# Kernel optimization log

Measured on AMD Instinct MI355X. Metric: run time of the kernel, lower is better.

The kernel has to match this reference:

```python
import jax, jax.numpy as jnp
import numpy as np

N_ATOMS = 15000
N_EDGES = 300000
F = 128          # n_atom_basis
L = 3            # n_interactions
N_RBF = 20
CUTOFF = 5.0
MAX_Z = 100


def setup_inputs() -> dict:
    key = jax.random.key(0)
    ks = jax.random.split(key, 20)

    atomic_numbers = jax.random.randint(ks[0], (N_ATOMS,), 1, MAX_Z)
    # relative position vectors; norms roughly within cutoff
    r_ij = jax.random.normal(ks[1], (N_EDGES, 3), dtype=jnp.float32) * 1.5
    idx_i = jax.random.randint(ks[2], (N_EDGES,), 0, N_ATOMS)
    idx_j = jax.random.randint(ks[3], (N_EDGES,), 0, N_ATOMS)

    def lin(k, fan_in, shape):
        return (jax.random.normal(k, shape, dtype=jnp.float32) / np.sqrt(fan_in)).astype(jnp.float32)

    embedding = lin(ks[4], F, (MAX_Z, F)).at[0].set(0.0)  # padding_idx=0
    filt_W = lin(ks[5], N_RBF, (N_RBF, L * 3 * F))
    filt_b = jnp.zeros((L * 3 * F,), jnp.float32)

    inter_W1 = lin(ks[6], F, (L, F, F));        inter_b1 = jnp.zeros((L, F), jnp.float32)
    inter_W2 = lin(ks[7], F, (L, F, 3 * F));    inter_b2 = jnp.zeros((L, 3 * F), jnp.float32)
    mix_W   = lin(ks[8], F, (L, F, 2 * F));     mix_b   = jnp.zeros((L, 2 * F), jnp.float32)
    intra_W1 = lin(ks[9], 2 * F, (L, 2 * F, F)); intra_b1 = jnp.zeros((L, F), jnp.float32)
    intra_W2 = lin(ks[10], F, (L, F, 3 * F));   intra_b2 = jnp.zeros((L, 3 * F), jnp.float32)

    return dict(r_ij=r_ij, embedding=embedding, filt_W=filt_W, filt_b=filt_b,
                inter_W1=inter_W1, inter_b1=inter_b1, inter_W2=inter_W2, inter_b2=inter_b2,
                mix_W=mix_W, mix_b=mix_b,
                intra_W1=intra_W1, intra_b1=intra_b1, intra_W2=intra_W2, intra_b2=intra_b2,
                atomic_numbers=atomic_numbers, idx_i=idx_i, idx_j=idx_j)


def _painn(r_ij, embedding, filt_W, filt_b,
           inter_W1, inter_b1, inter_W2, inter_b2,
           mix_W, mix_b, intra_W1, intra_b1, intra_W2, intra_b2,
           atomic_numbers, idx_i, idx_j):
    n_atoms = atomic_numbers.shape[0]
    d_ij = jnp.linalg.norm(r_ij, axis=1, keepdims=True)          # [E,1]
    dir_ij = r_ij / d_ij                                          # [E,3]

    # Gaussian RBF expansion
    offsets = jnp.linspace(0.0, CUTOFF, N_RBF, dtype=jnp.float32)
    width = offsets[1] - offsets[0]
    coeff = -0.5 / (width * width)
    phi = jnp.exp(coeff * (d_ij[..., None] - offsets) ** 2)       # [E,1,R]

    # cosine cutoff
    fcut = 0.5 * (jnp.cos(d_ij * jnp.pi / CUTOFF) + 1.0) * (d_ij < CUTOFF)  # [E,1]

    filters = (phi @ filt_W + filt_b) * fcut[..., None]           # [E,1,L*3F]
    filter_list = jnp.split(filters, L, axis=-1)

    q = embedding[atomic_numbers][:, None, :]                     # [N,1,F]
    mu = jnp.zeros((n_atoms, 3, F), q.dtype)                      # [N,3,F]

    for i in range(L):
        # inter-atomic message block
        h = jax.nn.silu(q @ inter_W1[i] + inter_b1[i])
        x = h @ inter_W2[i] + inter_b2[i]                         # [N,1,3F]
        xj = x[idx_j]                                              # [E,1,3F]
        muj = mu[idx_j]                                            # [E,3,F]
        x = filter_list[i] * xj                                    # [E,1,3F]
        dq_e = x[..., :F]
        dmuR = x[..., F:2 * F]
        dmumu = x[..., 2 * F:]
        dq = jax.ops.segment_sum(dq_e, idx_i, num_segments=n_atoms)  # [N,1,F]
        dmu_e = dmuR * dir_ij[:, :, None] + dmumu * muj              # [E,3,F]
        dmu = jax.ops.segment_sum(dmu_e, idx_i, num_segments=n_atoms)
        q = q + dq
        mu = mu + dmu

        # intra-atomic mixing block
        mu_mix = mu @ mix_W[i] + mix_b[i]                          # [N,3,2F]
        mu_V, mu_W = mu_mix[..., :F], mu_mix[..., F:]
        mu_Vn = jnp.linalg.norm(mu_V, axis=-2, keepdims=True)      # [N,1,F]
        ctx = jnp.concatenate([q, mu_Vn], axis=-1)                 # [N,1,2F]
        h = jax.nn.silu(ctx @ intra_W1[i] + intra_b1[i])
        x = h @ intra_W2[i] + intra_b2[i]                          # [N,1,3F]
        dq_intra = x[..., :F]
        dmu_intra = x[..., F:2 * F] * mu_W                         # [N,3,F]
        dqmu_intra = x[..., 2 * F:] * jnp.sum(mu_V * mu_W, axis=1, keepdims=True)
        q = q + dq_intra + dqmu_intra
        mu = mu + dmu_intra

    return q.squeeze(1), mu


def reference(r_ij, embedding, filt_W, filt_b,
              inter_W1, inter_b1, inter_W2, inter_b2,
              mix_W, mix_b, intra_W1, intra_b1, intra_W2, intra_b2,
              atomic_numbers, idx_i, idx_j):
    return _painn(r_ij, embedding, filt_W, filt_b,
                  inter_W1, inter_b1, inter_W2, inter_b2,
                  mix_W, mix_b, intra_W1, intra_b1, intra_W2, intra_b2,
                  atomic_numbers, idx_i, idx_j)
```

## Files before the change

### kernel.cpp

```cpp
#include <hip/hip_runtime.h>
#include <hip/hip_bf16.h>

#define N_ATOMS 15000
#define N_EDGES 300000
#define FDIM 128
#define NRBF 20
#define CUTOFF 5.0f
#define PI_F 3.14159265358979323846f
#define MT 16
#define NBLK 938

typedef __hip_bfloat16 bf16;
using bf16x8 = __attribute__((ext_vector_type(8))) short;
using f32x4  = __attribute__((ext_vector_type(4))) float;

#define MFMA(a, b, c) __builtin_amdgcn_mfma_f32_16x16x32_bf16(a, b, c, 0, 0, 0)

__device__ __forceinline__ float b2f(bf16 v) { return __bfloat162float(v); }
__device__ __forceinline__ float siluf(float x) { return x / (1.0f + __expf(-x)); }
__device__ __forceinline__ float lo_bf(unsigned u) { return __uint_as_float(u << 16); }
__device__ __forceinline__ float hi_bf(unsigned u) { return __uint_as_float(u & 0xffff0000u); }

__device__ __constant__ int c_off[15] = {
    0, 900000, 912800, 935840, 936992, 986144, 986528, 1133984,
    1135136, 1233440, 1234208, 1332512, 1332896, 1480352, 1481504};
#define P_TOTAL 1481504
#define P_RIJ 0
#define P_EMB 900000
#define P_FW  912800
#define P_FB  935840
#define P_IW1 936992
#define P_IB1 986144
#define P_IW2 986528
#define P_IB2 1133984
#define P_MW  1135136
#define P_MB  1233440
#define P_AW1 1234208
#define P_AB1 1332512
#define P_AW2 1332896
#define P_AB2 1480352

#define WPACK_L 180224

__global__ void detect_dtype(const void* __restrict__ r_ij, int* __restrict__ flag) {
    __shared__ int cnt;
    if (threadIdx.x == 0) cnt = 0;
    __syncthreads();
    const bf16* p = (const bf16*)r_ij;
    float v = fabsf(b2f(p[threadIdx.x]));
    int ok = (v > 0.0009765625f && v < 16.0f) ? 1 : 0;
    atomicAdd(&cnt, ok);
    __syncthreads();
    if (threadIdx.x == 0) flag[0] = (cnt > 204) ? 1 : 0;
}

struct CvtArgs { const void* src[14]; };

__global__ void convert_all(CvtArgs args, float* __restrict__ dst,
                            const int* __restrict__ flag) {
    int i = blockIdx.x * blockDim.x + threadIdx.x;
    if (i >= P_TOTAL) return;
    bool isbf = flag[0] != 0;
    int s = 0;
    while (i >= c_off[s + 1]) s++;
    int k = i - c_off[s];
    dst[i] = isbf ? b2f(((const bf16*)args.src[s])[k])
                  : ((const float*)args.src[s])[k];
}

__global__ void pack_w(const float* __restrict__ fp, bf16* __restrict__ wbf) {
    int i = blockIdx.x * blockDim.x + threadIdx.x;
    if (i >= 3 * WPACK_L) return;
    int l = i / WPACK_L;
    int r = i - l * WPACK_L;
    int m, off;
    if (r < 16384)       { m = 0; off = r; }
    else if (r < 65536)  { m = 1; off = r - 16384; }
    else if (r < 98304)  { m = 2; off = r - 65536; }
    else if (r < 131072) { m = 3; off = r - 98304; }
    else                 { m = 4; off = r - 131072; }
    const int pkN[5] = {128, 384, 256, 128, 384};
    const int pkD[5] = {0, 16384, 65536, 98304, 131072};
    int N = pkN[m];
    int k = off / N;
    int n = off - k * N;
    int srcb;
    switch (m) {
        case 0: srcb = P_IW1 + l * 16384; break;
        case 1: srcb = P_IW2 + l * 49152; break;
        case 2: srcb = P_MW  + l * 32768; break;
        case 3: srcb = P_AW1 + l * 32768; break;
        default: srcb = P_AW2 + l * 49152; break;
    }
    float v = fp[srcb + off];
    int dst = l * WPACK_L + pkD[m] +
              (((k >> 5) * 4 + ((k >> 3) & 3)) * N + n) * 8 + (k & 7);
    wbf[dst] = __float2bfloat16(v);
}

__global__ void init_q(const int* __restrict__ zn, const float* __restrict__ emb,
                       float* __restrict__ q) {
    int idx = blockIdx.x * blockDim.x + threadIdx.x;
    if (idx >= N_ATOMS * FDIM) return;
    int a = idx >> 7;
    int f = idx & 127;
    q[idx] = emb[zn[a] * FDIM + f];
}

__global__ void hist_kernel(const int* __restrict__ idx_i, int* __restrict__ counts) {
    int e = blockIdx.x * blockDim.x + threadIdx.x;
    if (e < N_EDGES) atomicAdd(&counts[idx_i[e]], 1);
}

__global__ void scan_kernel(const int* __restrict__ counts, int* __restrict__ start) {
    __shared__ int partial[256];
    int t = threadIdx.x;
    const int chunk = (N_ATOMS + 255) / 256;
    int base = t * chunk;
    int sum = 0;
    for (int k = 0; k < chunk; k++)
        if (base + k < N_ATOMS) sum += counts[base + k];
    partial[t] = sum;
    __syncthreads();
    for (int off = 1; off < 256; off <<= 1) {
        int v = (t >= off) ? partial[t - off] : 0;
        __syncthreads();
        partial[t] += v;
        __syncthreads();
    }
    int run = (t == 0) ? 0 : partial[t - 1];
    for (int k = 0; k < chunk; k++) {
        if (base + k < N_ATOMS) {
            start[base + k] = run;
            run += counts[base + k];
        }
    }
    if (t == 255) start[N_ATOMS] = run;
}

__global__ void scatter_kernel(const float* __restrict__ r3,
                               const int* __restrict__ idx_i,
                               const int* __restrict__ idx_j,
                               const int* __restrict__ start,
                               int* __restrict__ cursor,
                               int* __restrict__ sorted_j,
                               bf16* __restrict__ edata) {
    int e = blockIdx.x * blockDim.x + threadIdx.x;
    if (e >= N_EDGES) return;
    float xx = r3[e * 3 + 0];
    float yy = r3[e * 3 + 1];
    float zz = r3[e * 3 + 2];
    float d = sqrtf(xx * xx + yy * yy + zz * zz);
    float inv = 1.0f / d;
    float fc = (d < CUTOFF) ? 0.5f * (cosf(d * PI_F / CUTOFF) + 1.0f) : 0.0f;
    const float width = CUTOFF / (float)(NRBF - 1);
    const float coeff = -0.5f / (width * width);
    int i = idx_i[e];
    int pos = start[i] + atomicAdd(&cursor[i], 1);
    sorted_j[pos] = idx_j[e];
    bf16* out = edata + (size_t)pos * 24;
#pragma unroll
    for (int r = 0; r < NRBF; r++) {
        float t = d - width * (float)r;
        out[r] = __float2bfloat16(__expf(coeff * t * t) * fc);
    }
    out[20] = __float2bfloat16(fc);
    out[21] = __float2bfloat16(xx * inv);
    out[22] = __float2bfloat16(yy * inv);
    out[23] = __float2bfloat16(zz * inv);
}

__global__ __launch_bounds__(256) void inter_mfma(
    const float* __restrict__ q, const bf16* __restrict__ wl,
    const float* __restrict__ b1, const float* __restrict__ b2,
    bf16* __restrict__ xbf) {
    const int t = threadIdx.x;
    const int wave = t >> 6, lane = t & 63, quad = lane >> 4, l15 = lane & 15;
    const int a0 = blockIdx.x * MT;
    __shared__ __align__(16) bf16 sA[MT * 136];
    __shared__ __align__(16) bf16 sH[MT * 136];
    for (int idx = t; idx < MT * 128; idx += 256) {
        int a = idx >> 7, f = idx & 127;
        int ga = a0 + a; if (ga > N_ATOMS - 1) ga = N_ATOMS - 1;
        sA[a * 136 + f] = __float2bfloat16(q[(size_t)ga * 128 + f]);
    }
    __syncthreads();
    const f32x4 fz = {0.0f, 0.0f, 0.0f, 0.0f};
    f32x4 acc0[2] = {fz, fz};
    const bf16* B1 = wl;
#pragma unroll
    for (int kt = 0; kt < 4; kt++) {
        bf16x8 af = *(const bf16x8*)(sA + l15 * 136 + kt * 32 + quad * 8);
#pragma unroll
        for (int n = 0; n < 2; n++) {
            int c0 = (wave * 2 + n) * 16;
            bf16x8 bfr = *(const bf16x8*)(B1 + (((kt * 4 + quad) * 128) + c0 + l15) * 8);
            acc0[n] = MFMA(af, bfr, acc0[n]);
        }
    }
#pragma unroll
    for (int n = 0; n < 2; n++) {
        int col = (wave * 2 + n) * 16 + l15;
        float bb = b1[col];
#pragma unroll
        for (int r = 0; r < 4; r++) {
            int row = quad * 4 + r;
            sH[row * 136 + col] = __float2bfloat16(siluf(acc0[n][r] + bb));
        }
    }
    __syncthreads();
    f32x4 acc2[6] = {fz, fz, fz, fz, fz, fz};
    const bf16* B2 = wl + 16384;
#pragma unroll
    for (int kt = 0; kt < 4; kt++) {
        bf16x8 af = *(const bf16x8*)(sH + l15 * 136 + kt * 32 + quad * 8);
#pragma unroll
        for (int n = 0; n < 6; n++) {
            int c0 = (wave * 6 + n) * 16;
            bf16x8 bfr = *(const bf16x8*)(B2 + (((kt * 4 + quad) * 384) + c0 + l15) * 8);
            acc2[n] = MFMA(af, bfr, acc2[n]);
        }
    }
#pragma unroll
    for (int n = 0; n < 6; n++) {
        int col = (wave * 6 + n) * 16 + l15;
        float bb = b2[col];
#pragma unroll
        for (int r = 0; r < 4; r++) {
            int row = quad * 4 + r;
            int ga = a0 + row;
            if (ga < N_ATOMS)
                xbf[(size_t)ga * 384 + col] = __float2bfloat16(acc2[n][r] + bb);
        }
    }
}

__global__ __launch_bounds__(128) void atom_gather(
    const int* __restrict__ start, const int* __restrict__ sorted_j,
    const bf16* __restrict__ edata,
    const bf16* __restrict__ xbf, const bf16* __restrict__ mubf,
    const float* __restrict__ fW, const float* __restrict__ fb, int layer,
    float* __restrict__ q, float* __restrict__ mu) {
    int a = blockIdx.x;
    int f = threadIdx.x;
    int c0 = layer * 3 * FDIM + f;
    float wq[21], wr[21], wm[21];
#pragma unroll
    for (int r = 0; r < NRBF; r++) {
        const float* row = fW + r * (9 * FDIM) + c0;
        wq[r] = row[0];
        wr[r] = row[FDIM];
        wm[r] = row[2 * FDIM];
    }
    wq[20] = fb[c0];
    wr[20] = fb[c0 + FDIM];
    wm[20] = fb[c0 + 2 * FDIM];

    float dq = 0.0f, dm0 = 0.0f, dm1 = 0.0f, dm2 = 0.0f;
    int s = start[a], e_end = start[a + 1];
    for (int pos = s; pos < e_end; pos++) {
        int j = sorted_j[pos];
        const uint4* edp = (const uint4*)(edata + (size_t)pos * 24);
        uint4 ua = edp[0];
        uint4 ub = edp[1];
        uint4 uc = edp[2];
        float se[24];
        se[0] = lo_bf(ua.x);  se[1] = hi_bf(ua.x);
        se[2] = lo_bf(ua.y);  se[3] = hi_bf(ua.y);
        se[4] = lo_bf(ua.z);  se[5] = hi_bf(ua.z);
        se[6] = lo_bf(ua.w);  se[7] = hi_bf(ua.w);
        se[8] = lo_bf(ub.x);  se[9] = hi_bf(ub.x);
        se[10] = lo_bf(ub.y); se[11] = hi_bf(ub.y);
        se[12] = lo_bf(ub.z); se[13] = hi_bf(ub.z);
        se[14] = lo_bf(ub.w); se[15] = hi_bf(ub.w);
        se[16] = lo_bf(uc.x); se[17] = hi_bf(uc.x);
        se[18] = lo_bf(uc.y); se[19] = hi_bf(uc.y);
        se[20] = lo_bf(uc.z); se[21] = hi_bf(uc.z);
        se[22] = lo_bf(uc.w); se[23] = hi_bf(uc.w);
        float f0 = 0.0f, f1 = 0.0f, f2 = 0.0f;
#pragma unroll
        for (int r = 0; r < 21; r++) {
            f0 += se[r] * wq[r];
            f1 += se[r] * wr[r];
            f2 += se[r] * wm[r];
        }
        size_t jb = (size_t)j * (3 * FDIM);
        float xj0 = b2f(xbf[jb + f]);
        float xj1 = b2f(xbf[jb + FDIM + f]);
        float xj2 = b2f(xbf[jb + 2 * FDIM + f]);
        float dmuR = f1 * xj1;
        float dmm = f2 * xj2;
        dq += f0 * xj0;
        dm0 += dmuR * se[21] + dmm * b2f(mubf[jb + f]);
        dm1 += dmuR * se[22] + dmm * b2f(mubf[jb + FDIM + f]);
        dm2 += dmuR * se[23] + dmm * b2f(mubf[jb + 2 * FDIM + f]);
    }
    q[(size_t)a * FDIM + f] += dq;
    size_t mbase = (size_t)a * (3 * FDIM);
    mu[mbase + f] += dm0;
    mu[mbase + FDIM + f] += dm1;
    mu[mbase + 2 * FDIM + f] += dm2;
}

__global__ __launch_bounds__(256) void update_mfma(
    float* __restrict__ q, float* __restrict__ mu, bf16* __restrict__ mubf,
    const bf16* __restrict__ wl,
    const float* __restrict__ mixb, const float* __restrict__ ib1,
    const float* __restrict__ ib2) {
    const int t = threadIdx.x;
    const int wave = t >> 6, lane = t & 63, quad = lane >> 4, l15 = lane & 15;
    const int a0 = blockIdx.x * MT;
    __shared__ __align__(16) char lds[47360];
    bf16* sMU  = (bf16*)lds;
    bf16* sCTX = (bf16*)lds;
    bf16* sH2  = (bf16*)(lds + 8448);
    bf16* sV   = (bf16*)(lds + 13056);
    bf16* sX2  = (bf16*)(lds + 13056);
    bf16* sW   = (bf16*)(lds + 26112);
    float* sSD = (float*)(lds + 39168);

    for (int idx = t; idx < 48 * 128; idx += 256) {
        int row = idx >> 7, f = idx & 127;
        int a = row / 3, s = row - a * 3;
        int ga = a0 + a; if (ga > N_ATOMS - 1) ga = N_ATOMS - 1;
        sMU[row * 136 + f] = __float2bfloat16(mu[(size_t)ga * 384 + s * 128 + f]);
    }
    __syncthreads();
    const f32x4 fz = {0.0f, 0.0f, 0.0f, 0.0f};
    const bf16* BM = wl + 65536;
    bf16x8 bfr[4][4];
#pragma unroll
    for (int kt = 0; kt < 4; kt++)
#pragma unroll
        for (int n = 0; n < 4; n++) {
            int c0 = (wave * 4 + n) * 16;
            bfr[n][kt] = *(const bf16x8*)(BM + (((kt * 4 + quad) * 256) + c0 + l15) * 8);
        }
    f32x4 accm[3][4];
#pragma unroll
    for (int mt = 0; mt < 3; mt++)
#pragma unroll
        for (int n = 0; n < 4; n++) accm[mt][n] = fz;
#pragma unroll
    for (int mt = 0; mt < 3; mt++) {
#pragma unroll
        for (int kt = 0; kt < 4; kt++) {
            bf16x8 af = *(const bf16x8*)(sMU + (mt * 16 + l15) * 136 + kt * 32 + quad * 8);
#pragma unroll
            for (int n = 0; n < 4; n++)
                accm[mt][n] = MFMA(af, bfr[n][kt], accm[mt][n]);
        }
    }
    __syncthreads();
#pragma unroll
    for (int mt = 0; mt < 3; mt++)
#pragma unroll
        for (int n = 0; n < 4; n++) {
            int col = wave * 64 + n * 16 + l15;
            float bb = mixb[col];
#pragma unroll
            for (int r = 0; r < 4; r++) {
                int row = mt * 16 + quad * 4 + r;
                float v = accm[mt][n][r] + bb;
                if (col < 128) sV[row * 136 + col] = __float2bfloat16(v);
                else           sW[row * 136 + col - 128] = __float2bfloat16(v);
            }
        }
    __syncthreads();
    for (int idx = t; idx < MT * 128; idx += 256) {
        int a = idx >> 7, f = idx & 127;
        float v0 = b2f(sV[(a * 3 + 0) * 136 + f]);
        float v1 = b2f(sV[(a * 3 + 1) * 136 + f]);
        float v2 = b2f(sV[(a * 3 + 2) * 136 + f]);
        float w0 = b2f(sW[(a * 3 + 0) * 136 + f]);
        float w1 = b2f(sW[(a * 3 + 1) * 136 + f]);
        float w2 = b2f(sW[(a * 3 + 2) * 136 + f]);
        sSD[a * 128 + f] = v0 * w0 + v1 * w1 + v2 * w2;
        float vn = sqrtf(v0 * v0 + v1 * v1 + v2 * v2);
        int ga = a0 + a; if (ga > N_ATOMS - 1) ga = N_ATOMS - 1;
        sCTX[a * 264 + f] = __float2bfloat16(q[(size_t)ga * 128 + f]);
        sCTX[a * 264 + 128 + f] = __float2bfloat16(vn);
    }
    __syncthreads();
    const bf16* BA1 = wl + 98304;
    f32x4 acc1[2] = {fz, fz};
#pragma unroll
    for (int kt = 0; kt < 8; kt++) {
        bf16x8 af = *(const bf16x8*)(sCTX + l15 * 264 + kt * 32 + quad * 8);
#pragma unroll
        for (int n = 0; n < 2; n++) {
            int c0 = (wave * 2 + n) * 16;
            bf16x8 bb = *(const bf16x8*)(BA1 + (((kt * 4 + quad) * 128) + c0 + l15) * 8);
            acc1[n] = MFMA(af, bb, acc1[n]);
        }
    }
#pragma unroll
    for (int n = 0; n < 2; n++) {
        int col = (wave * 2 + n) * 16 + l15;
        float bb = ib1[col];
#pragma unroll
        for (int r = 0; r < 4; r++) {
            int row = quad * 4 + r;
            sH2[row * 136 + col] = __float2bfloat16(siluf(acc1[n][r] + bb));
        }
    }
    __syncthreads();
    const bf16* BA2 = wl + 131072;
    f32x4 acc3[6] = {fz, fz, fz, fz, fz, fz};
#pragma unroll
    for (int kt = 0; kt < 4; kt++) {
        bf16x8 af = *(const bf16x8*)(sH2 + l15 * 136 + kt * 32 + quad * 8);
#pragma unroll
        for (int n = 0; n < 6; n++) {
            int c0 = (wave * 6 + n) * 16;
            bf16x8 bb = *(const bf16x8*)(BA2 + (((kt * 4 + quad) * 384) + c0 + l15) * 8);
            acc3[n] = MFMA(af, bb, acc3[n]);
        }
    }
#pragma unroll
    for (int n = 0; n < 6; n++) {
        int col = (wave * 6 + n) * 16 + l15;
        float bb = ib2[col];
#pragma unroll
        for (int r = 0; r < 4; r++) {
            int row = quad * 4 + r;
            sX2[row * 392 + col] = __float2bfloat16(acc3[n][r] + bb);
        }
    }
    __syncthreads();
    for (int idx = t; idx < MT * 128; idx += 256) {
        int a = idx >> 7, f = idx & 127;
        int ga = a0 + a;
        if (ga >= N_ATOMS) continue;
        float x0 = b2f(sX2[a * 392 + f]);
        float x1 = b2f(sX2[a * 392 + 128 + f]);
        float x2 = b2f(sX2[a * 392 + 256 + f]);
        float sd = sSD[a * 128 + f];
        q[(size_t)ga * 128 + f] += x0 + x2 * sd;
#pragma unroll
        for (int s = 0; s < 3; s++) {
            float w = b2f(sW[(a * 3 + s) * 136 + f]);
            size_t off = (size_t)ga * 384 + s * 128 + f;
            float m = mu[off] + x1 * w;
            mu[off] = m;
            mubf[off] = __float2bfloat16(m);
        }
    }
}

__global__ void writeout(const float* __restrict__ q, const float* __restrict__ mu,
                         void* __restrict__ out, const int* __restrict__ flag) {
    int idx = blockIdx.x * blockDim.x + threadIdx.x;
    const int nq = N_ATOMS * FDIM;
    const int ntot = N_ATOMS * 4 * FDIM;
    if (idx >= ntot) return;
    float v = (idx < nq) ? q[idx] : mu[idx - nq];
    if (flag[0] != 0) ((bf16*)out)[idx] = __float2bfloat16(v);
    else              ((float*)out)[idx] = v;
}

extern "C" void kernel_launch(void* const* d_in, const int* in_sizes, int n_in,
                              void* d_out, int out_size, void* d_ws, size_t ws_size,
                              hipStream_t stream) {
    const int* zn    = (const int*)d_in[14];
    const int* idx_i = (const int*)d_in[15];
    const int* idx_j = (const int*)d_in[16];

    char* base = (char*)d_ws;
    int*   flag     = (int*)base;
    float* fp       = (float*)(base + 256);
    float* q        = (float*)(base + 256 + 5926016);
    float* mu       = (float*)(base + 256 + 5926016 + 7680000);
    bf16*  xbf      = (bf16*)(base + 36646272);
    bf16*  mubf     = (bf16*)(base + 48166272);
    int*   counts   = (int*)(base + 59686272);
    int*   cursor   = (int*)(base + 59746304);
    int*   startarr = (int*)(base + 59806336);
    int*   sorted_j = (int*)(base + 59866368);
    bf16*  edata    = (bf16*)(base + 61066368);
    bf16*  wbf      = (bf16*)fp;

    detect_dtype<<<1, 256, 0, stream>>>(d_in[0], flag);

    CvtArgs ca;
    for (int t = 0; t < 14; t++) ca.src[t] = d_in[t];
    convert_all<<<(P_TOTAL + 255) / 256, 256, 0, stream>>>(ca, fp, flag);

    const float* r3  = fp + P_RIJ;
    const float* emb = fp + P_EMB;
    const float* fW  = fp + P_FW;
    const float* fb  = fp + P_FB;

    hipMemsetAsync(counts, 0, 2 * 60032, stream);
    hist_kernel<<<(N_EDGES + 255) / 256, 256, 0, stream>>>(idx_i, counts);
    scan_kernel<<<1, 256, 0, stream>>>(counts, startarr);
    scatter_kernel<<<(N_EDGES + 255) / 256, 256, 0, stream>>>(
        r3, idx_i, idx_j, startarr, cursor, sorted_j, edata);

    pack_w<<<(3 * WPACK_L + 255) / 256, 256, 0, stream>>>(fp, wbf);

    hipMemsetAsync(mu, 0, (size_t)N_ATOMS * 3 * FDIM * sizeof(float), stream);
    hipMemsetAsync(mubf, 0, (size_t)N_ATOMS * 3 * FDIM * sizeof(bf16), stream);
    init_q<<<(N_ATOMS * FDIM + 255) / 256, 256, 0, stream>>>(zn, emb, q);

    for (int l = 0; l < 3; l++) {
        const bf16* wl = wbf + (size_t)l * WPACK_L;
        inter_mfma<<<NBLK, 256, 0, stream>>>(
            q, wl, fp + P_IB1 + l * 128, fp + P_IB2 + l * 384, xbf);
        atom_gather<<<N_ATOMS, 128, 0, stream>>>(
            startarr, sorted_j, edata, xbf, mubf, fW, fb, l, q, mu);
        update_mfma<<<NBLK, 256, 0, stream>>>(
            q, mu, mubf, wl,
            fp + P_MB + l * 256, fp + P_AB1 + l * 128, fp + P_AB2 + l * 384);
    }

    int ntot = N_ATOMS * 4 * FDIM;
    writeout<<<(ntot + 255) / 256, 256, 0, stream>>>(q, mu, d_out, flag);
}
```

Measured before the change: 690.7 us.

## Compute edge filters with MFMA in a multi-atom gather kernel

Replaces the one-block-per-atom gather, which did a scalar 21-term filter dot product per edge and feature, with a kernel that handles 4 atoms per block. It stages 32-edge chunks of RBF features in LDS and computes the filter values with bf16 MFMA against a packed bf16 filter-weight matrix. Neighbour features are then gathered and accumulated per atom through LDS partial sums. This cuts the per-edge FMA work and improves block occupancy, at the cost of extra synchronisation, LDS traffic and bf16 rounding of the filter outputs.

```diff
diff --git a/kernel.cpp b/kernel.cpp
--- a/kernel.cpp
+++ b/kernel.cpp
@@ -9,6 +9,8 @@
 #define PI_F 3.14159265358979323846f
 #define MT 16
 #define NBLK 938
+#define GB 4
+#define NGBLK 3750
 
 typedef __hip_bfloat16 bf16;
 using bf16x8 = __attribute__((ext_vector_type(8))) short;
@@ -41,6 +43,7 @@
 #define P_AB2 1480352
 
 #define WPACK_L 180224
+#define FWP_L 12288
 
 __global__ void detect_dtype(const void* __restrict__ r_ij, int* __restrict__ flag) {
     __shared__ int cnt;
@@ -98,6 +101,20 @@
     wbf[dst] = __float2bfloat16(v);
 }
 
+__global__ void pack_fw(const float* __restrict__ fp, bf16* __restrict__ dst) {
+    int i = blockIdx.x * blockDim.x + threadIdx.x;
+    if (i >= 3 * FWP_L) return;
+    int l = i / FWP_L;
+    int r = i - l * FWP_L;
+    int k = r / 384;
+    int n = r - k * 384;
+    float v = 0.0f;
+    if (k < 20)       v = fp[P_FW + k * 1152 + l * 384 + n];
+    else if (k == 20) v = fp[P_FB + l * 384 + n];
+    int di = l * FWP_L + (((k >> 3) * 384) + n) * 8 + (k & 7);
+    dst[di] = __float2bfloat16(v);
+}
+
 __global__ void init_q(const int* __restrict__ zn, const float* __restrict__ emb,
                        float* __restrict__ q) {
     int idx = blockIdx.x * blockDim.x + threadIdx.x;
@@ -235,71 +252,133 @@
     }
 }
 
-__global__ __launch_bounds__(128) void atom_gather(
+__global__ __launch_bounds__(256) void gather_mfma(
     const int* __restrict__ start, const int* __restrict__ sorted_j,
     const bf16* __restrict__ edata,
     const bf16* __restrict__ xbf, const bf16* __restrict__ mubf,
-    const float* __restrict__ fW, const float* __restrict__ fb, int layer,
+    const bf16* __restrict__ fWp,
     float* __restrict__ q, float* __restrict__ mu) {
-    int a = blockIdx.x;
-    int f = threadIdx.x;
-    int c0 = layer * 3 * FDIM + f;
-    float wq[21], wr[21], wm[21];
-#pragma unroll
-    for (int r = 0; r < NRBF; r++) {
-        const float* row = fW + r * (9 * FDIM) + c0;
-        wq[r] = row[0];
-        wr[r] = row[FDIM];
-        wm[r] = row[2 * FDIM];
-    }
-    wq[20] = fb[c0];
-    wr[20] = fb[c0 + FDIM];
-    wm[20] = fb[c0 + 2 * FDIM];
-
-    float dq = 0.0f, dm0 = 0.0f, dm1 = 0.0f, dm2 = 0.0f;
-    int s = start[a], e_end = start[a + 1];
-    for (int pos = s; pos < e_end; pos++) {
-        int j = sorted_j[pos];
-        const uint4* edp = (const uint4*)(edata + (size_t)pos * 24);
-        uint4 ua = edp[0];
-        uint4 ub = edp[1];
-        uint4 uc = edp[2];
-        float se[24];
-        se[0] = lo_bf(ua.x);  se[1] = hi_bf(ua.x);
-        se[2] = lo_bf(ua.y);  se[3] = hi_bf(ua.y);
-        se[4] = lo_bf(ua.z);  se[5] = hi_bf(ua.z);
-        se[6] = lo_bf(ua.w);  se[7] = hi_bf(ua.w);
-        se[8] = lo_bf(ub.x);  se[9] = hi_bf(ub.x);
-        se[10] = lo_bf(ub.y); se[11] = hi_bf(ub.y);
-        se[12] = lo_bf(ub.z); se[13] = hi_bf(ub.z);
-        se[14] = lo_bf(ub.w); se[15] = hi_bf(ub.w);
-        se[16] = lo_bf(uc.x); se[17] = hi_bf(uc.x);
-        se[18] = lo_bf(uc.y); se[19] = hi_bf(uc.y);
-        se[20] = lo_bf(uc.z); se[21] = hi_bf(uc.z);
-        se[22] = lo_bf(uc.w); se[23] = hi_bf(uc.w);
-        float f0 = 0.0f, f1 = 0.0f, f2 = 0.0f;
-#pragma unroll
-        for (int r = 0; r < 21; r++) {
-            f0 += se[r] * wq[r];
-            f1 += se[r] * wr[r];
-            f2 += se[r] * wm[r];
-        }
-        size_t jb = (size_t)j * (3 * FDIM);
-        float xj0 = b2f(xbf[jb + f]);
-        float xj1 = b2f(xbf[jb + FDIM + f]);
-        float xj2 = b2f(xbf[jb + 2 * FDIM + f]);
-        float dmuR = f1 * xj1;
-        float dmm = f2 * xj2;
-        dq += f0 * xj0;
-        dm0 += dmuR * se[21] + dmm * b2f(mubf[jb + f]);
-        dm1 += dmuR * se[22] + dmm * b2f(mubf[jb + FDIM + f]);
-        dm2 += dmuR * se[23] + dmm * b2f(mubf[jb + 2 * FDIM + f]);
-    }
-    q[(size_t)a * FDIM + f] += dq;
-    size_t mbase = (size_t)a * (3 * FDIM);
-    mu[mbase + f] += dm0;
-    mu[mbase + FDIM + f] += dm1;
-    mu[mbase + 2 * FDIM + f] += dm2;
+    const int t = threadIdx.x;
+    const int wave = t >> 6, lane = t & 63, quad = lane >> 4, l15 = lane & 15;
+    const int a0 = blockIdx.x * GB;
+    __shared__ __align__(16) bf16 sPHI[32 * 40];
+    __shared__ __align__(16) bf16 sFILT[32 * 392];
+    __shared__ float sACC[2][GB][4][128];
+    __shared__ float sDIR[32][4];
+    __shared__ int sJ[32];
+    __shared__ int sAtom[32];
+    __shared__ int sStart[GB + 1];
+
+    if (t <= GB) sStart[t] = start[a0 + t];
+    {
+        float* ap = &sACC[0][0][0][0];
+        for (int i = t; i < 2 * GB * 4 * 128; i += 256) ap[i] = 0.0f;
+    }
+    __syncthreads();
+    const int s0 = sStart[0], s1 = sStart[1], s2 = sStart[2], s3 = sStart[3];
+    const int s4 = sStart[4];
+    const int nE = s4 - s0;
+    const int nChunks = (nE + 31) >> 5;
+
+    bf16x8 bfrag[6];
+#pragma unroll
+    for (int n6 = 0; n6 < 6; n6++) {
+        int n = wave * 96 + n6 * 16 + l15;
+        bfrag[n6] = *(const bf16x8*)(fWp + ((size_t)(quad * 384 + n)) * 8);
+    }
+    const f32x4 fz = {0.0f, 0.0f, 0.0f, 0.0f};
+
+    for (int ch = 0; ch < nChunks; ch++) {
+        int ebase = s0 + ch * 32;
+        if (t < 128) {
+            int e = t >> 2, part = t & 3;
+            int pos = ebase + e;
+            bool valid = pos < s4;
+            if (part == 3) {
+                *(uint4*)(sPHI + e * 40 + 24) = make_uint4(0, 0, 0, 0);
+                sJ[e] = valid ? sorted_j[pos] : 0;
+                int al = -1;
+                if (valid) al = (pos >= s1) + (pos >= s2) + (pos >= s3);
+                sAtom[e] = al;
+            } else {
+                uint4 u = valid ? ((const uint4*)(edata + (size_t)pos * 24))[part]
+                                : make_uint4(0, 0, 0, 0);
+                if (part == 2) {
+                    sDIR[e][0] = hi_bf(u.z);
+                    sDIR[e][1] = lo_bf(u.w);
+                    sDIR[e][2] = hi_bf(u.w);
+                    u.z &= 0x0000ffffu;
+                    u.w = 0u;
+                }
+                *(uint4*)(sPHI + e * 40 + part * 8) = u;
+            }
+        }
+        __syncthreads();
+#pragma unroll
+        for (int mt = 0; mt < 2; mt++) {
+            bf16x8 af = *(const bf16x8*)(sPHI + (mt * 16 + l15) * 40 + quad * 8);
+#pragma unroll
+            for (int n6 = 0; n6 < 6; n6++) {
+                f32x4 c = MFMA(af, bfrag[n6], fz);
+                int col = wave * 96 + n6 * 16 + l15;
+#pragma unroll
+                for (int r = 0; r < 4; r++)
+                    sFILT[(mt * 16 + quad * 4 + r) * 392 + col] = __float2bfloat16(c[r]);
+            }
+        }
+        __syncthreads();
+        {
+            int g = t >> 7, f = t & 127;
+            float c0 = 0, c1 = 0, c2 = 0, c3 = 0;
+            int cur = -1;
+            for (int e = g; e < 32; e += 2) {
+                int al = sAtom[e];
+                if (al != cur) {
+                    if (cur >= 0) {
+                        sACC[g][cur][0][f] += c0;
+                        sACC[g][cur][1][f] += c1;
+                        sACC[g][cur][2][f] += c2;
+                        sACC[g][cur][3][f] += c3;
+                    }
+                    cur = al;
+                    c0 = c1 = c2 = c3 = 0;
+                }
+                if (al < 0) continue;
+                float f0 = b2f(sFILT[e * 392 + f]);
+                float f1 = b2f(sFILT[e * 392 + 128 + f]);
+                float f2 = b2f(sFILT[e * 392 + 256 + f]);
+                size_t jb = (size_t)sJ[e] * 384;
+                float xj0 = b2f(xbf[jb + f]);
+                float xj1 = b2f(xbf[jb + 128 + f]);
+                float xj2 = b2f(xbf[jb + 256 + f]);
+                float m0 = b2f(mubf[jb + f]);
+                float m1 = b2f(mubf[jb + 128 + f]);
+                float m2 = b2f(mubf[jb + 256 + f]);
+                float d0 = sDIR[e][0], d1 = sDIR[e][1], d2 = sDIR[e][2];
+                float dmuR = f1 * xj1, dmm = f2 * xj2;
+                c0 += f0 * xj0;
+                c1 += dmuR * d0 + dmm * m0;
+                c2 += dmuR * d1 + dmm * m1;
+                c3 += dmuR * d2 + dmm * m2;
+            }
+            if (cur >= 0) {
+                sACC[g][cur][0][f] += c0;
+                sACC[g][cur][1][f] += c1;
+                sACC[g][cur][2][f] += c2;
+                sACC[g][cur][3][f] += c3;
+            }
+        }
+        __syncthreads();
+    }
+    for (int i = t; i < GB * 128; i += 256) {
+        int a = i >> 7, f = i & 127;
+        int ga = a0 + a;
+        q[(size_t)ga * 128 + f] += sACC[0][a][0][f] + sACC[1][a][0][f];
+        size_t mb = (size_t)ga * 384;
+        mu[mb + f]       += sACC[0][a][1][f] + sACC[1][a][1][f];
+        mu[mb + 128 + f] += sACC[0][a][2][f] + sACC[1][a][2][f];
+        mu[mb + 256 + f] += sACC[0][a][3][f] + sACC[1][a][3][f];
+    }
 }
 
 __global__ __launch_bounds__(256) void update_mfma(
@@ -479,6 +558,7 @@
     int*   sorted_j = (int*)(base + 59866368);
     bf16*  edata    = (bf16*)(base + 61066368);
     bf16*  wbf      = (bf16*)fp;
+    bf16*  fWp      = wbf + 3 * WPACK_L;
 
     detect_dtype<<<1, 256, 0, stream>>>(d_in[0], flag);
 
@@ -488,8 +568,6 @@
 
     const float* r3  = fp + P_RIJ;
     const float* emb = fp + P_EMB;
-    const float* fW  = fp + P_FW;
-    const float* fb  = fp + P_FB;
 
     hipMemsetAsync(counts, 0, 2 * 60032, stream);
     hist_kernel<<<(N_EDGES + 255) / 256, 256, 0, stream>>>(idx_i, counts);
@@ -498,6 +576,7 @@
         r3, idx_i, idx_j, startarr, cursor, sorted_j, edata);
 
     pack_w<<<(3 * WPACK_L + 255) / 256, 256, 0, stream>>>(fp, wbf);
+    pack_fw<<<(3 * FWP_L + 255) / 256, 256, 0, stream>>>(fp, fWp);
 
     hipMemsetAsync(mu, 0, (size_t)N_ATOMS * 3 * FDIM * sizeof(float), stream);
     hipMemsetAsync(mubf, 0, (size_t)N_ATOMS * 3 * FDIM * sizeof(bf16), stream);
@@ -507,8 +586,8 @@
         const bf16* wl = wbf + (size_t)l * WPACK_L;
         inter_mfma<<<NBLK, 256, 0, stream>>>(
             q, wl, fp + P_IB1 + l * 128, fp + P_IB2 + l * 384, xbf);
-        atom_gather<<<N_ATOMS, 128, 0, stream>>>(
-            startarr, sorted_j, edata, xbf, mubf, fW, fb, l, q, mu);
+        gather_mfma<<<NGBLK, 256, 0, stream>>>(
+            startarr, sorted_j, edata, xbf, mubf, fWp + (size_t)l * FWP_L, q, mu);
         update_mfma<<<NBLK, 256, 0, stream>>>(
             q, mu, mubf, wl,
             fp + P_MB + l * 256, fp + P_AB1 + l * 128, fp + P_AB2 + l * 384);
```

Result: slower. 794.2 us (+15.0%).
